# Kernel tuning notes

Hardware: AMD Instinct MI355X
Metric: run time of the kernel (lower is better)

The kernel has to match this reference:

```python
import jax, jax.numpy as jnp
import numpy as np

DROPOUT = 0.1      # ban radius in normalized coords
INVALID = -2.0     # PositionGetter.INVALID sentinel
EPS = 1e-08


def setup_inputs() -> dict:
    key = jax.random.key(0)
    k1, k2, k3 = jax.random.split(key, 3)
    B, C, T, D = 64, 275, 3000, 2
    x = jax.random.normal(k1, (B, C, T), dtype=jnp.float32)
    positions = jax.random.uniform(k2, (B, C, D), dtype=jnp.float32)
    # row 0: the ban center applied to x; rows 1..100: Monte-Carlo test centers
    centers = jax.random.uniform(k3, (101, D), dtype=jnp.float32)
    return {"x": x, "positions": positions, "centers": centers}


def reference(x, positions, centers):
    # valid_mask: channel is valid unless all coords equal the INVALID sentinel
    valid = ~jnp.all(positions == INVALID, axis=-1)          # [B, C] bool
    x = x * valid[..., None].astype(x.dtype)
    # distances from every channel position to every center, all at once
    # centers: [N, D], positions: [B, C, D] -> dist: [N, B, C]
    diff = positions[None, :, :, :] - centers[:, None, None, :]
    dist = jnp.linalg.norm(diff, axis=-1)                    # [N, B, C]
    kept_all = (dist > DROPOUT) | (~valid)[None]             # [N, B, C] bool
    # apply the actual ban (first center)
    x = x * kept_all[0][..., None].astype(x.dtype)
    # Monte-Carlo keep probability over the remaining 100 centers
    prob_kept = jnp.mean(kept_all[1:].astype(x.dtype), axis=0)  # [B, C]
    return x / (prob_kept[..., None] + EPS)
```

## Files before the change

kernel.cpp:

```cpp
#include <hip/hip_runtime.h>
#include <math.h>


typedef float f32x4 __attribute__((ext_vector_type(4)));

__global__ __launch_bounds__(256) void ChannelDropout_scales_kernel(
    const float* __restrict__ pos,
    const float* __restrict__ centers,
    float* __restrict__ scale,
    int rows, int ncenters)
{
    const int wid  = (int)((blockIdx.x * 256u + threadIdx.x) >> 6);
    const int lane = threadIdx.x & 63;
    if (wid >= rows) return;

    const float px = pos[2 * wid];
    const float py = pos[2 * wid + 1];
    const bool valid = !(px == -2.0f && py == -2.0f);

    float cnt = 0.0f;
    for (int c = 1 + lane; c < ncenters; c += 64) {
        const float dx = px - centers[2 * c];
        const float dy = py - centers[2 * c + 1];
        const float d2 = __fadd_rn(__fmul_rn(dx, dx), __fmul_rn(dy, dy));
        cnt += (sqrtf(d2) > 0.1f) ? 1.0f : 0.0f;
    }
    #pragma unroll
    for (int off = 32; off > 0; off >>= 1)
        cnt += __shfl_xor(cnt, off, 64);

    if (lane == 0) {
        const float dx0 = px - centers[0];
        const float dy0 = py - centers[1];
        const float d02 = __fadd_rn(__fmul_rn(dx0, dx0), __fmul_rn(dy0, dy0));
        const bool kept0 = sqrtf(d02) > 0.1f;
        const int denom = (ncenters > 1) ? (ncenters - 1) : 1;
        const float prob = cnt / (float)denom;
        scale[wid] = (valid && kept0) ? (1.0f / (prob + 1e-8f)) : 0.0f;
    }
}

__global__ __launch_bounds__(256) void ChannelDropout_apply_kernel(
    const float* __restrict__ x,
    const float* __restrict__ scale,
    float* __restrict__ out,
    int rows, int tlen)
{
    const int tid = threadIdx.x;
    const int t4  = tlen >> 2;
    for (int row = blockIdx.x; row < rows; row += gridDim.x) {
        const float s = scale[row];
        const size_t base = (size_t)row * (size_t)tlen;
        const f32x4* __restrict__ xr   = (const f32x4*)(x + base);
        f32x4* __restrict__       orow = (f32x4*)(out + base);
        for (int i = tid; i < t4; i += 256) {
            f32x4 v = xr[i];
            __builtin_nontemporal_store(v * s, orow + i);
        }
        for (int i = (t4 << 2) + tid; i < tlen; i += 256) {
            out[base + i] = x[base + i] * s;
        }
    }
}

__global__ __launch_bounds__(256) void ChannelDropout_fused_kernel(
    const float* __restrict__ x,
    const float* __restrict__ pos,
    const float* __restrict__ centers,
    float* __restrict__ out,
    int ncenters, int tlen)
{
    const int row  = blockIdx.x;
    const int tid  = threadIdx.x;
    const int lane = tid & 63;

    const float px = pos[2 * row];
    const float py = pos[2 * row + 1];
    const bool valid = !(px == -2.0f && py == -2.0f);
    float cnt = 0.0f;
    for (int c = 1 + lane; c < ncenters; c += 64) {
        const float dx = px - centers[2 * c];
        const float dy = py - centers[2 * c + 1];
        const float d2 = __fadd_rn(__fmul_rn(dx, dx), __fmul_rn(dy, dy));
        cnt += (sqrtf(d2) > 0.1f) ? 1.0f : 0.0f;
    }
    #pragma unroll
    for (int off = 32; off > 0; off >>= 1)
        cnt += __shfl_xor(cnt, off, 64);
    const float dx0 = px - centers[0];
    const float dy0 = py - centers[1];
    const float d02 = __fadd_rn(__fmul_rn(dx0, dx0), __fmul_rn(dy0, dy0));
    const bool kept0 = sqrtf(d02) > 0.1f;
    const int denom = (ncenters > 1) ? (ncenters - 1) : 1;
    const float prob = cnt / (float)denom;
    const float s = (valid && kept0) ? (1.0f / (prob + 1e-8f)) : 0.0f;

    const size_t base = (size_t)row * (size_t)tlen;
    const int t4 = tlen >> 2;
    const f32x4* __restrict__ xr   = (const f32x4*)(x + base);
    f32x4* __restrict__       orow = (f32x4*)(out + base);
    for (int i = tid; i < t4; i += 256) {
        f32x4 v = xr[i];
        __builtin_nontemporal_store(v * s, orow + i);
    }
    for (int i = (t4 << 2) + tid; i < tlen; i += 256)
        out[base + i] = x[base + i] * s;
}

extern "C" void kernel_launch(void* const* d_in, const int* in_sizes, int n_in,
                              void* d_out, int out_size, void* d_ws, size_t ws_size,
                              hipStream_t stream) {
    const float* x       = (const float*)d_in[0];
    const float* pos     = (const float*)d_in[1];
    const float* centers = (const float*)d_in[2];
    float* out = (float*)d_out;

    const int rows     = in_sizes[1] / 2;
    const int tlen     = in_sizes[0] / rows;
    const int ncenters = in_sizes[2] / 2;

    if (d_ws != nullptr && ws_size >= (size_t)rows * sizeof(float)) {
        float* scale = (float*)d_ws;
        const int ablocks = (rows + 3) / 4;
        ChannelDropout_scales_kernel<<<ablocks, 256, 0, stream>>>(
            pos, centers, scale, rows, ncenters);
        const int bblocks = 2048;
        ChannelDropout_apply_kernel<<<bblocks, 256, 0, stream>>>(
            x, scale, out, rows, tlen);
    } else {
        ChannelDropout_fused_kernel<<<rows, 256, 0, stream>>>(
            x, pos, centers, out, ncenters, tlen);
    }
}
```

Baseline: 374.9 us.

## Flatten apply kernel into grid-stride float4 loop with magic-number row division

```diff
diff --git a/kernel.cpp b/kernel.cpp
--- a/kernel.cpp
+++ b/kernel.cpp
@@ -40,26 +40,48 @@
     }
 }
 
-__global__ __launch_bounds__(256) void ChannelDropout_apply_kernel(
+__global__ __launch_bounds__(256) void ChannelDropout_apply_flat(
     const float* __restrict__ x,
     const float* __restrict__ scale,
     float* __restrict__ out,
-    int rows, int tlen)
+    int n4, unsigned long long magic)
 {
-    const int tid = threadIdx.x;
-    const int t4  = tlen >> 2;
-    for (int row = blockIdx.x; row < rows; row += gridDim.x) {
-        const float s = scale[row];
-        const size_t base = (size_t)row * (size_t)tlen;
-        const f32x4* __restrict__ xr   = (const f32x4*)(x + base);
-        f32x4* __restrict__       orow = (f32x4*)(out + base);
-        for (int i = tid; i < t4; i += 256) {
-            f32x4 v = xr[i];
-            __builtin_nontemporal_store(v * s, orow + i);
-        }
-        for (int i = (t4 << 2) + tid; i < tlen; i += 256) {
-            out[base + i] = x[base + i] * s;
-        }
+    const f32x4* __restrict__ x4 = (const f32x4*)x;
+    f32x4* __restrict__       o4 = (f32x4*)out;
+    const int nt = (int)(gridDim.x * blockDim.x);
+    int i = (int)(blockIdx.x * blockDim.x + threadIdx.x);
+
+    for (; i + 3 * nt < n4; i += 4 * nt) {
+        const int i0 = i, i1 = i + nt, i2 = i + 2 * nt, i3 = i + 3 * nt;
+        const f32x4 v0 = x4[i0];
+        const f32x4 v1 = x4[i1];
+        const f32x4 v2 = x4[i2];
+        const f32x4 v3 = x4[i3];
+        const float s0 = scale[(int)(((unsigned long long)(unsigned)i0 * magic) >> 40)];
+        const float s1 = scale[(int)(((unsigned long long)(unsigned)i1 * magic) >> 40)];
+        const float s2 = scale[(int)(((unsigned long long)(unsigned)i2 * magic) >> 40)];
+        const float s3 = scale[(int)(((unsigned long long)(unsigned)i3 * magic) >> 40)];
+        o4[i0] = v0 * s0;
+        o4[i1] = v1 * s1;
+        o4[i2] = v2 * s2;
+        o4[i3] = v3 * s3;
+    }
+    for (; i < n4; i += nt) {
+        const float s = scale[(int)(((unsigned long long)(unsigned)i * magic) >> 40)];
+        o4[i] = x4[i] * s;
+    }
+}
+
+__global__ __launch_bounds__(256) void ChannelDropout_apply_scalar(
+    const float* __restrict__ x,
+    const float* __restrict__ scale,
+    float* __restrict__ out,
+    long long n, int tlen)
+{
+    const long long nt = (long long)gridDim.x * blockDim.x;
+    for (long long i = (long long)blockIdx.x * blockDim.x + threadIdx.x;
+         i < n; i += nt) {
+        out[i] = x[i] * scale[(int)(i / tlen)];
     }
 }
 
@@ -101,7 +123,7 @@
     f32x4* __restrict__       orow = (f32x4*)(out + base);
     for (int i = tid; i < t4; i += 256) {
         f32x4 v = xr[i];
-        __builtin_nontemporal_store(v * s, orow + i);
+        orow[i] = v * s;
     }
     for (int i = (t4 << 2) + tid; i < tlen; i += 256)
         out[base + i] = x[base + i] * s;
@@ -118,15 +140,31 @@
     const int rows     = in_sizes[1] / 2;
     const int tlen     = in_sizes[0] / rows;
     const int ncenters = in_sizes[2] / 2;
+    if (rows <= 0 || tlen <= 0) return;
 
     if (d_ws != nullptr && ws_size >= (size_t)rows * sizeof(float)) {
         float* scale = (float*)d_ws;
         const int ablocks = (rows + 3) / 4;
         ChannelDropout_scales_kernel<<<ablocks, 256, 0, stream>>>(
             pos, centers, scale, rows, ncenters);
+
         const int bblocks = 2048;
-        ChannelDropout_apply_kernel<<<bblocks, 256, 0, stream>>>(
-            x, scale, out, rows, tlen);
+        if ((tlen & 3) == 0) {
+            const int t4r = tlen >> 2;
+            const long long n4 = (long long)rows * t4r;
+            const unsigned long long magic = (0x10000000000ULL / (unsigned)t4r) + 1ULL;
+            const bool magic_ok =
+                (double)t4r * (double)n4 < 1.0e12 &&
+                (double)n4 * (double)magic < 1.8e19;
+            if (magic_ok && n4 < 2147000000LL) {
+                ChannelDropout_apply_flat<<<bblocks, 256, 0, stream>>>(
+                    x, scale, out, (int)n4, magic);
+                return;
+            }
+        }
+        const long long n = (long long)rows * tlen;
+        ChannelDropout_apply_scalar<<<bblocks, 256, 0, stream>>>(
+            x, scale, out, n, tlen);
     } else {
         ChannelDropout_fused_kernel<<<rows, 256, 0, stream>>>(
             x, pos, centers, out, ncenters, tlen);
```

Measured after the change: 370.4 us. No clear change (-1.2%).
